# Kernel optimization log

Measured on AMD Instinct MI355X. Metric: run time of the kernel, lower is better.

Reference implementation:

```python
import jax, jax.numpy as jnp
import numpy as np

KERNEL_SIZES = (3, 5, 7)
NUM_HEAD = 6
DIM = 192
K_SCALES = 3
HEADS_PER_SCALE = NUM_HEAD // K_SCALES  # 2
HEAD_DIM = DIM // NUM_HEAD              # 32
SCALE = HEAD_DIM ** -0.5


def _nbr_idx(L, K):
    # NATTEN non-causal, dilation=1: window centered on query, clamped at edges.
    start = jnp.clip(jnp.arange(L) - K // 2, 0, L - K)
    return start[:, None] + jnp.arange(K)  # [L, K]


def _na3d_branch(xi, K):
    # xi: [B, D, H, W, C] with C = 3 * HEADS_PER_SCALE * HEAD_DIM
    B, D, H, W, C = xi.shape
    qkv = xi.reshape(B, D, H, W, 3, HEADS_PER_SCALE, HEAD_DIM).transpose(4, 0, 5, 1, 2, 3, 6)
    q, k, v = qkv[0] * SCALE, qkv[1], qkv[2]  # each [B, h, D, H, W, hd]

    idd, idh, idw = _nbr_idx(D, K), _nbr_idx(H, K), _nbr_idx(W, K)

    def gather(t):
        t = jnp.take(t, idd, axis=2)  # [B,h,D,K,H,W,hd]
        t = jnp.take(t, idh, axis=4)  # [B,h,D,K,H,K,W,hd]
        t = jnp.take(t, idw, axis=6)  # [B,h,D,K,H,K,W,K,hd]
        return t

    kn = gather(k)
    vn = gather(v)
    # attention logits over the K^3 neighborhood per query
    attn = jnp.einsum('bndhwc,bndihjwkc->bndhwijk', q, kn)
    attn = jax.nn.softmax(attn.reshape(B, HEADS_PER_SCALE, D, H, W, K ** 3), axis=-1)
    attn = attn.reshape(B, HEADS_PER_SCALE, D, H, W, K, K, K)
    y = jnp.einsum('bndhwijk,bndihjwkc->bndhwc', attn, vn)
    # [B,h,D,H,W,hd] -> [B,D,H,W,h*hd]
    return y.transpose(0, 2, 3, 4, 1, 5).reshape(B, D, H, W, HEADS_PER_SCALE * HEAD_DIM)


def setup_inputs() -> dict:
    key = jax.random.key(0)
    k0, k1, k2 = jax.random.split(key, 3)
    x = jax.random.normal(k0, (1, 8, 24, 24, DIM), dtype=jnp.float32)
    W_qkv = jax.random.normal(k1, (DIM, 3 * DIM), dtype=jnp.float32) * 0.02
    b_qkv = jnp.zeros((3 * DIM,), dtype=jnp.float32)
    W_proj = jax.random.normal(k2, (DIM, DIM), dtype=jnp.float32) * 0.02
    b_proj = jnp.zeros((DIM,), dtype=jnp.float32)
    return {'x': x, 'W_qkv': W_qkv, 'b_qkv': b_qkv, 'W_proj': W_proj, 'b_proj': b_proj}


def reference(x, W_qkv, b_qkv, W_proj, b_proj):
    qkv = x @ W_qkv + b_qkv  # [B,D,H,W,3*DIM]
    # torch.split with channels [DIM, DIM, DIM]
    chunks = jnp.split(qkv, K_SCALES, axis=4)
    ys = [_na3d_branch(chunks[i], KERNEL_SIZES[i]) for i in range(K_SCALES)]
    y = jnp.concatenate(ys, axis=4)  # [B,D,H,W,DIM]
    return y @ W_proj + b_proj
```

## Files before the change

### kernel.cpp

```cpp
#include <hip/hip_runtime.h>

typedef unsigned short ushort_t;
typedef unsigned int uint_t;
typedef __attribute__((ext_vector_type(8))) short short8;
typedef __attribute__((ext_vector_type(4))) float f32x4;

constexpr int DD = 8, HH = 24, WW = 24;
constexpr int NQ = DD * HH * WW;
constexpr int CIN = 192;
constexpr int CQKV = 576;
constexpr int KP = 576;
constexpr float ATT_SCALE = 0.17677669529663687f;
constexpr int NROW = DD * HH;

__device__ __forceinline__ ushort_t bf16h(float x) {
    uint_t u = __float_as_uint(x);
    u += 0x7FFFu + ((u >> 16) & 1u);
    return (ushort_t)(u >> 16);
}
__device__ __forceinline__ float bf16f(ushort_t h) {
    return __uint_as_float(((uint_t)h) << 16);
}
__device__ __forceinline__ float2 unpack2(uint_t u) {
    return make_float2(__uint_as_float(u << 16),
                       __uint_as_float(u & 0xffff0000u));
}
__device__ __forceinline__ float quad_add_xor1(float x) {
    return x + __int_as_float(__builtin_amdgcn_mov_dpp(__float_as_int(x), 0xB1, 0xF, 0xF, true));
}
__device__ __forceinline__ float quad_add_xor2(float x) {
    return x + __int_as_float(__builtin_amdgcn_mov_dpp(__float_as_int(x), 0x4E, 0xF, 0xF, true));
}

constexpr int EB0 = 0;
constexpr int EB1 = NROW * 2 * WW * 2;
constexpr int EB2 = EB1 + NROW * 3 * WW * 2;
constexpr int ETOT = EB2 + NROW * 4 * WW * 2;

__global__ __launch_bounds__(256)
void convert_w_kernel(const float* __restrict__ Wq, const float* __restrict__ Wp,
                      ushort_t* __restrict__ Bq, ushort_t* __restrict__ Bp)
{
    __shared__ float T[32][36];
    int b = blockIdx.x;
    const float* W; ushort_t* Bb; int N;
    int kt, nt;
    if (b < 108) { W = Wq; Bb = Bq; N = CQKV; kt = b % 6; nt = b / 6; }
    else         { b -= 108; W = Wp; Bb = Bp; N = CIN; kt = b % 6; nt = b / 6; }
    const int k0 = kt * 32, n0 = nt * 32;
    const int tid = threadIdx.x;

    #pragma unroll
    for (int p = 0; p < 4; ++p) {
        int e = p * 256 + tid;
        int r = e >> 5, c = e & 31;
        T[c][r] = W[(long)(k0 + r) * N + n0 + c];
    }
    __syncthreads();
    const int n = tid >> 3;
    const int k4 = (tid & 7) * 4;
    float4 v = *(const float4*)(&T[n][k4]);
    ushort4 hv, lv;
    hv.x = bf16h(v.x); lv.x = bf16h(v.x - bf16f(hv.x));
    hv.y = bf16h(v.y); lv.y = bf16h(v.y - bf16f(hv.y));
    hv.z = bf16h(v.z); lv.z = bf16h(v.z - bf16f(hv.z));
    hv.w = bf16h(v.w); lv.w = bf16h(v.w - bf16f(hv.w));
    const int k = k0 + k4;
    const int g = k >> 6;
    const int kc = k & 63;
    ushort_t* row = Bb + (long)(n0 + n) * KP + g * 192 + kc;
    *(ushort4*)(row)       = hv;
    *(ushort4*)(row + 64)  = lv;
    *(ushort4*)(row + 128) = hv;
}

__global__ __launch_bounds__(256)
void gemm_mfma_kernel(const float* __restrict__ A, const ushort_t* __restrict__ Bb,
                      const float* __restrict__ bias, ushort_t* __restrict__ Cout, int N)
{
    __shared__ ushort_t As[64][72];
    __shared__ ushort_t Bs[64][72];
    __shared__ float Ct[64][68];

    const int tid = threadIdx.x;
    const int bm = blockIdx.x * 64;
    const int bn = blockIdx.y * 64;

    const int wv = tid >> 6;
    const int lane = tid & 63;
    const int lm = lane & 15;
    const int quad = lane >> 4;
    const int wr = (wv >> 1) * 32;
    const int wc = (wv & 1) * 32;

    const int ar = tid >> 4;
    const int ac4 = (tid & 15) * 4;
    const int br0 = tid >> 3;
    const int bc0 = (tid & 7) * 8;

    f32x4 acc[2][2] = {};

    float4 av[4];
    #pragma unroll
    for (int p = 0; p < 4; ++p)
        av[p] = *(const float4*)(A + (long)(bm + ar + p * 16) * CIN + ac4);
    uint4 nb0 = *(const uint4*)(Bb + (long)(bn + br0) * KP + bc0);
    uint4 nb1 = *(const uint4*)(Bb + (long)(bn + br0 + 32) * KP + bc0);

    #pragma unroll
    for (int g = 0; g < 3; ++g) {
        ushort4 hv4[4];
        #pragma unroll
        for (int ph = 0; ph < 3; ++ph) {
            const uint4 b0 = nb0, b1 = nb1;
            __syncthreads();
            if (ph == 0) {
                #pragma unroll
                for (int p = 0; p < 4; ++p) {
                    float4 v = av[p];
                    ushort4 hv;
                    hv.x = bf16h(v.x); hv.y = bf16h(v.y);
                    hv.z = bf16h(v.z); hv.w = bf16h(v.w);
                    hv4[p] = hv;
                    *(ushort4*)(&As[ar + p * 16][ac4]) = hv;
                }
            } else if (ph == 2) {
                #pragma unroll
                for (int p = 0; p < 4; ++p) {
                    float4 v = av[p];
                    ushort4 lv;
                    lv.x = bf16h(v.x - bf16f(hv4[p].x));
                    lv.y = bf16h(v.y - bf16f(hv4[p].y));
                    lv.z = bf16h(v.z - bf16f(hv4[p].z));
                    lv.w = bf16h(v.w - bf16f(hv4[p].w));
                    *(ushort4*)(&As[ar + p * 16][ac4]) = lv;
                }
            }
            *(uint4*)(&Bs[br0][bc0]) = b0;
            *(uint4*)(&Bs[br0 + 32][bc0]) = b1;
            const int nidx = g * 3 + ph + 1;
            if (nidx < 9) {
                const int nkk = (nidx / 3) * 192 + (nidx % 3) * 64;
                nb0 = *(const uint4*)(Bb + (long)(bn + br0) * KP + nkk + bc0);
                nb1 = *(const uint4*)(Bb + (long)(bn + br0 + 32) * KP + nkk + bc0);
            }
            if (ph == 2 && g < 2) {
                #pragma unroll
                for (int p = 0; p < 4; ++p)
                    av[p] = *(const float4*)(A + (long)(bm + ar + p * 16) * CIN + (g + 1) * 64 + ac4);
            }
            __syncthreads();

            #pragma unroll
            for (int ks = 0; ks < 64; ks += 32) {
                short8 af0 = *(const short8*)(&As[wr + lm][ks + quad * 8]);
                short8 af1 = *(const short8*)(&As[wr + 16 + lm][ks + quad * 8]);
                short8 bf0 = *(const short8*)(&Bs[wc + lm][ks + quad * 8]);
                short8 bf1 = *(const short8*)(&Bs[wc + 16 + lm][ks + quad * 8]);
                acc[0][0] = __builtin_amdgcn_mfma_f32_16x16x32_bf16(af0, bf0, acc[0][0], 0, 0, 0);
                acc[0][1] = __builtin_amdgcn_mfma_f32_16x16x32_bf16(af0, bf1, acc[0][1], 0, 0, 0);
                acc[1][0] = __builtin_amdgcn_mfma_f32_16x16x32_bf16(af1, bf0, acc[1][0], 0, 0, 0);
                acc[1][1] = __builtin_amdgcn_mfma_f32_16x16x32_bf16(af1, bf1, acc[1][1], 0, 0, 0);
            }
        }
    }

    #pragma unroll
    for (int tc = 0; tc < 2; ++tc) {
        const float bv = bias[bn + wc + tc * 16 + lm];
        #pragma unroll
        for (int tr = 0; tr < 2; ++tr) {
            #pragma unroll
            for (int reg = 0; reg < 4; ++reg)
                Ct[wr + tr * 16 + quad * 4 + reg][wc + tc * 16 + lm] = acc[tr][tc][reg] + bv;
        }
    }
    __syncthreads();
    const int orow = tid >> 4;
    const int oc4 = (tid & 15) * 4;
    #pragma unroll
    for (int p = 0; p < 4; ++p) {
        const int r = orow + p * 16;
        float4 v = *(const float4*)(&Ct[r][oc4]);
        ushort4 hv;
        hv.x = bf16h(v.x); hv.y = bf16h(v.y); hv.z = bf16h(v.z); hv.w = bf16h(v.w);
        *(ushort4*)(Cout + (long)(bm + r) * N + bn + oc4) = hv;
    }
}

__global__ __launch_bounds__(256)
void gemm_proj_kernel(const float* __restrict__ accs, const float* __restrict__ stats,
                      const ushort_t* __restrict__ Bb, const float* __restrict__ bias,
                      float* __restrict__ Cout)
{
    __shared__ ushort_t As[64][72];
    __shared__ ushort_t Bs[64][72];
    __shared__ float Ct[64][68];

    const int tid = threadIdx.x;
    const int bm = blockIdx.x * 64;
    const int bn = blockIdx.y * 64;

    const int wv = tid >> 6;
    const int lane = tid & 63;
    const int lm = lane & 15;
    const int quad = lane >> 4;
    const int wr = (wv >> 1) * 32;
    const int wc = (wv & 1) * 32;

    const int ar = tid >> 4;
    const int ac4 = (tid & 15) * 4;
    const int a_hd = ac4 >> 5;
    const int a_cc = ac4 & 31;
    const int br0 = tid >> 3;
    const int bc0 = (tid & 7) * 8;

    f32x4 acc[2][2] = {};

    auto load_av = [&](int gg, float4* av) {
        const int CK = gg + 2;
        const int eb = (gg == 0) ? EB0 : (gg == 1 ? EB1 : EB2);
        #pragma unroll
        for (int p = 0; p < 4; ++p) {
            const int q = bm + ar + p * 16;
            const int rr = q / WW;
            const int w = q - rr * WW;
            const int e0 = eb + (rr * CK) * (WW * 2) + w * 2 + a_hd;
            float S = 0.f;
            float4 a = make_float4(0.f, 0.f, 0.f, 0.f);
            #pragma unroll
            for (int c = 0; c < 4; ++c) {
                if (c < CK) {
                    const int e = e0 + c * (WW * 2);
                    S += stats[e];
                    const float4 t = *(const float4*)(accs + (long)e * 32 + a_cc);
                    a.x += t.x; a.y += t.y; a.z += t.z; a.w += t.w;
                }
            }
            const float rs = 1.0f / S;
            av[p] = make_float4(a.x * rs, a.y * rs, a.z * rs, a.w * rs);
        }
    };

    float4 av[4];
    load_av(0, av);
    uint4 nb0 = *(const uint4*)(Bb + (long)(bn + br0) * KP + bc0);
    uint4 nb1 = *(const uint4*)(Bb + (long)(bn + br0 + 32) * KP + bc0);

    #pragma unroll
    for (int g = 0; g < 3; ++g) {
        ushort4 hv4[4];
        #pragma unroll
        for (int ph = 0; ph < 3; ++ph) {
            const uint4 b0 = nb0, b1 = nb1;
            __syncthreads();
            if (ph == 0) {
                #pragma unroll
                for (int p = 0; p < 4; ++p) {
                    float4 v = av[p];
                    ushort4 hv;
                    hv.x = bf16h(v.x); hv.y = bf16h(v.y);
                    hv.z = bf16h(v.z); hv.w = bf16h(v.w);
                    hv4[p] = hv;
                    *(ushort4*)(&As[ar + p * 16][ac4]) = hv;
                }
            } else if (ph == 2) {
                #pragma unroll
                for (int p = 0; p < 4; ++p) {
                    float4 v = av[p];
                    ushort4 lv;
                    lv.x = bf16h(v.x - bf16f(hv4[p].x));
                    lv.y = bf16h(v.y - bf16f(hv4[p].y));
                    lv.z = bf16h(v.z - bf16f(hv4[p].z));
                    lv.w = bf16h(v.w - bf16f(hv4[p].w));
                    *(ushort4*)(&As[ar + p * 16][ac4]) = lv;
                }
            }
            *(uint4*)(&Bs[br0][bc0]) = b0;
            *(uint4*)(&Bs[br0 + 32][bc0]) = b1;
            const int nidx = g * 3 + ph + 1;
            if (nidx < 9) {
                const int nkk = (nidx / 3) * 192 + (nidx % 3) * 64;
                nb0 = *(const uint4*)(Bb + (long)(bn + br0) * KP + nkk + bc0);
                nb1 = *(const uint4*)(Bb + (long)(bn + br0 + 32) * KP + nkk + bc0);
            }
            if (ph == 2 && g < 2)
                load_av(g + 1, av);
            __syncthreads();

            #pragma unroll
            for (int ks = 0; ks < 64; ks += 32) {
                short8 af0 = *(const short8*)(&As[wr + lm][ks + quad * 8]);
                short8 af1 = *(const short8*)(&As[wr + 16 + lm][ks + quad * 8]);
                short8 bf0 = *(const short8*)(&Bs[wc + lm][ks + quad * 8]);
                short8 bf1 = *(const short8*)(&Bs[wc + 16 + lm][ks + quad * 8]);
                acc[0][0] = __builtin_amdgcn_mfma_f32_16x16x32_bf16(af0, bf0, acc[0][0], 0, 0, 0);
                acc[0][1] = __builtin_amdgcn_mfma_f32_16x16x32_bf16(af0, bf1, acc[0][1], 0, 0, 0);
                acc[1][0] = __builtin_amdgcn_mfma_f32_16x16x32_bf16(af1, bf0, acc[1][0], 0, 0, 0);
                acc[1][1] = __builtin_amdgcn_mfma_f32_16x16x32_bf16(af1, bf1, acc[1][1], 0, 0, 0);
            }
        }
    }

    #pragma unroll
    for (int tc = 0; tc < 2; ++tc) {
        const float bv = bias[bn + wc + tc * 16 + lm];
        #pragma unroll
        for (int tr = 0; tr < 2; ++tr) {
            #pragma unroll
            for (int reg = 0; reg < 4; ++reg)
                Ct[wr + tr * 16 + quad * 4 + reg][wc + tc * 16 + lm] = acc[tr][tc][reg] + bv;
        }
    }
    __syncthreads();
    const int orow = tid >> 4;
    const int oc4 = (tid & 15) * 4;
    #pragma unroll
    for (int p = 0; p < 4; ++p) {
        const int r = orow + p * 16;
        float4 v = *(const float4*)(&Ct[r][oc4]);
        *(float4*)(Cout + (long)(bm + r) * CIN + bn + oc4) = v;
    }
}

constexpr int KROW = 72;
constexpr int RBUF = WW * KROW;

template<int K>
__device__ __forceinline__
void split_chunk(const ushort_t* __restrict__ qkv,
                 float* __restrict__ accs, float* __restrict__ stats,
                 int r, int c, int nchunks, int scale, int ebase,
                 int w, int hd, int d8, int tid,
                 ushort_t* __restrict__ ksh, ushort_t* __restrict__ vsh)
{
    const int i0 = 2 * c;
    const int ni = (K - i0) < 2 ? (K - i0) : 2;
    const int NT = ni * K;

    const int dq = r / HH, hq = r % HH;
    int sd = dq - K / 2; sd = sd < 0 ? 0 : (sd > DD - K ? DD - K : sd);
    int sh = hq - K / 2; sh = sh < 0 ? 0 : (sh > HH - K ? HH - K : sh);
    int sw = w  - K / 2; sw = sw < 0 ? 0 : (sw > WW - K ? WW - K : sw);

    const int q = (dq * HH + hq) * WW + w;

    uint4 qu = *(const uint4*)(qkv + (long)q * CQKV + scale * 192 + hd * 32 + d8 * 8);
    float2 qf[4] = {unpack2(qu.x), unpack2(qu.y), unpack2(qu.z), unpack2(qu.w)};
    #pragma unroll
    for (int t = 0; t < 4; ++t) {
        qf[t].x *= ATT_SCALE;
        qf[t].y *= ATT_SCALE;
    }

    const int lw = tid >> 3;
    const int c8 = (tid & 7) * 8;

    auto src_ptr = [&](int t) {
        int i = i0 + t / K;
        int j = t - (t / K) * K;
        return qkv + (long)(((sd + i) * HH + (sh + j)) * WW + lw) * CQKV
             + scale * 192 + c8;
    };

    uint4 ck, cv;
    {
        const ushort_t* p0 = src_ptr(0);
        uint4 k0 = *(const uint4*)(p0 + 64);
        uint4 v0 = *(const uint4*)(p0 + 128);
        const ushort_t* p1 = src_ptr(1);
        ck = *(const uint4*)(p1 + 64);
        cv = *(const uint4*)(p1 + 128);
        *(uint4*)(ksh + lw * KROW + c8) = k0;
        *(uint4*)(vsh + lw * KROW + c8) = v0;
    }

    float sum = 0.f;
    float2 acc[4] = {};
    const int choff = hd * 32 + d8 * 8;

    for (int t = 0; t < NT; ++t) {
        __syncthreads();
        uint4 nk, nv;
        const bool issue = (t + 2 < NT);
        if (issue) {
            const ushort_t* pn = src_ptr(t + 2);
            nk = *(const uint4*)(pn + 64);
            nv = *(const uint4*)(pn + 128);
        }

        const ushort_t* kb = ksh + (t % 3) * RBUF + choff;
        const ushort_t* vb = vsh + (t % 3) * RBUF + choff;
        #pragma unroll
        for (int n = 0; n < K; ++n) {
            uint4 ku = *(const uint4*)(kb + (sw + n) * KROW);
            float2 k0 = unpack2(ku.x), k1 = unpack2(ku.y),
                   k2 = unpack2(ku.z), k3 = unpack2(ku.w);
            float2 d;
            d.x  = qf[0].x * k0.x; d.y  = qf[0].y * k0.y;
            d.x += qf[1].x * k1.x; d.y += qf[1].y * k1.y;
            d.x += qf[2].x * k2.x; d.y += qf[2].y * k2.y;
            d.x += qf[3].x * k3.x; d.y += qf[3].y * k3.y;
            float p = d.x + d.y;
            p = quad_add_xor1(p);
            p = quad_add_xor2(p);
            float pr = __expf(p);
            sum += pr;
            uint4 vu = *(const uint4*)(vb + (sw + n) * KROW);
            float2 v0 = unpack2(vu.x), v1 = unpack2(vu.y),
                   v2 = unpack2(vu.z), v3 = unpack2(vu.w);
            acc[0].x += pr * v0.x; acc[0].y += pr * v0.y;
            acc[1].x += pr * v1.x; acc[1].y += pr * v1.y;
            acc[2].x += pr * v2.x; acc[2].y += pr * v2.y;
            acc[3].x += pr * v3.x; acc[3].y += pr * v3.y;
        }

        if (t + 1 < NT) {
            *(uint4*)(ksh + ((t + 1) % 3) * RBUF + lw * KROW + c8) = ck;
            *(uint4*)(vsh + ((t + 1) % 3) * RBUF + lw * KROW + c8) = cv;
        }
        ck = nk; cv = nv;
    }

    const int e = ebase + ((r * nchunks + c) * WW + w) * 2 + hd;
    if (d8 == 0) stats[e] = sum;
    float* ap = accs + (long)e * 32 + d8 * 8;
    *(float4*)(ap)     = make_float4(acc[0].x, acc[0].y, acc[1].x, acc[1].y);
    *(float4*)(ap + 4) = make_float4(acc[2].x, acc[2].y, acc[3].x, acc[3].y);
}

__global__ __launch_bounds__(192)
void na3d_split_kernel(const ushort_t* __restrict__ qkv,
                       float* __restrict__ accs, float* __restrict__ stats)
{
    __shared__ alignas(16) ushort_t ksh[3 * RBUF];
    __shared__ alignas(16) ushort_t vsh[3 * RBUF];

    const int tid = threadIdx.x;
    const int w  = tid >> 3;
    const int hd = (tid >> 2) & 1;
    const int d8 = tid & 3;

    const int orig = blockIdx.x;
    int bid;
    if (orig < NROW * 4) {
        bid = (orig & 7) * (NROW * 4 / 8) + (orig >> 3);
    } else if (orig < NROW * 7) {
        const int t = orig - NROW * 4;
        bid = NROW * 4 + (t & 7) * (NROW * 3 / 8) + (t >> 3);
    } else {
        const int t = orig - NROW * 7;
        bid = NROW * 7 + (t & 7) * (NROW * 2 / 8) + (t >> 3);
    }

    if (bid < NROW * 4) {
        int r = bid >> 2, c = bid & 3;
        split_chunk<7>(qkv, accs, stats, r, c, 4, 2, EB2, w, hd, d8, tid, ksh, vsh);
    } else if (bid < NROW * 4 + NROW * 3) {
        int t = bid - NROW * 4;
        int r = t / 3, c = t - (t / 3) * 3;
        split_chunk<5>(qkv, accs, stats, r, c, 3, 1, EB1, w, hd, d8, tid, ksh, vsh);
    } else {
        int t = bid - NROW * 7;
        int r = t >> 1, c = t & 1;
        split_chunk<3>(qkv, accs, stats, r, c, 2, 0, EB0, w, hd, d8, tid, ksh, vsh);
    }
}

extern "C" void kernel_launch(void* const* d_in, const int* in_sizes, int n_in,
                              void* d_out, int out_size, void* d_ws, size_t ws_size,
                              hipStream_t stream)
{
    const float* x      = (const float*)d_in[0];
    const float* W_qkv  = (const float*)d_in[1];
    const float* b_qkv  = (const float*)d_in[2];
    const float* W_proj = (const float*)d_in[3];
    const float* b_proj = (const float*)d_in[4];
    float* out = (float*)d_out;

    float* accs    = (float*)d_ws;
    float* stats   = accs + (long)ETOT * 32;
    ushort_t* qkvb = (ushort_t*)(stats + ETOT);
    ushort_t* Wbq  = qkvb + (long)NQ * CQKV;
    ushort_t* Wbp  = Wbq + (long)CQKV * KP;

    convert_w_kernel<<<dim3(144), 256, 0, stream>>>(W_qkv, W_proj, Wbq, Wbp);

    gemm_mfma_kernel<<<dim3(NQ / 64, CQKV / 64), 256, 0, stream>>>(x, Wbq, b_qkv, qkvb, CQKV);

    na3d_split_kernel<<<dim3(NROW * (4 + 3 + 2)), 192, 0, stream>>>(qkvb, accs, stats);

    gemm_proj_kernel<<<dim3(NQ / 64, CIN / 64), 256, 0, stream>>>(accs, stats, Wbp, b_proj, out);
}
```

Before: 110.4 us.

## Fuse weight conversion into QKV GEMM and use fp16 dot2 in attention

```diff
diff --git a/kernel.cpp b/kernel.cpp
--- a/kernel.cpp
+++ b/kernel.cpp
@@ -3,7 +3,9 @@
 typedef unsigned short ushort_t;
 typedef unsigned int uint_t;
 typedef __attribute__((ext_vector_type(8))) short short8;
+typedef __attribute__((ext_vector_type(8))) unsigned short ushort8;
 typedef __attribute__((ext_vector_type(4))) float f32x4;
+typedef __attribute__((ext_vector_type(2))) _Float16 half2v;
 
 constexpr int DD = 8, HH = 24, WW = 24;
 constexpr int NQ = DD * HH * WW;
@@ -21,9 +23,9 @@
 __device__ __forceinline__ float bf16f(ushort_t h) {
     return __uint_as_float(((uint_t)h) << 16);
 }
-__device__ __forceinline__ float2 unpack2(uint_t u) {
-    return make_float2(__uint_as_float(u << 16),
-                       __uint_as_float(u & 0xffff0000u));
+__device__ __forceinline__ ushort_t f16h(float x) {
+    _Float16 h = (_Float16)x;
+    return __builtin_bit_cast(ushort_t, h);
 }
 __device__ __forceinline__ float quad_add_xor1(float x) {
     return x + __int_as_float(__builtin_amdgcn_mov_dpp(__float_as_int(x), 0xB1, 0xF, 0xF, true));
@@ -38,133 +40,164 @@
 constexpr int ETOT = EB2 + NROW * 4 * WW * 2;
 
 __global__ __launch_bounds__(256)
-void convert_w_kernel(const float* __restrict__ Wq, const float* __restrict__ Wp,
-                      ushort_t* __restrict__ Bq, ushort_t* __restrict__ Bp)
-{
-    __shared__ float T[32][36];
-    int b = blockIdx.x;
-    const float* W; ushort_t* Bb; int N;
-    int kt, nt;
-    if (b < 108) { W = Wq; Bb = Bq; N = CQKV; kt = b % 6; nt = b / 6; }
-    else         { b -= 108; W = Wp; Bb = Bp; N = CIN; kt = b % 6; nt = b / 6; }
-    const int k0 = kt * 32, n0 = nt * 32;
-    const int tid = threadIdx.x;
-
-    #pragma unroll
-    for (int p = 0; p < 4; ++p) {
-        int e = p * 256 + tid;
-        int r = e >> 5, c = e & 31;
-        T[c][r] = W[(long)(k0 + r) * N + n0 + c];
-    }
-    __syncthreads();
-    const int n = tid >> 3;
-    const int k4 = (tid & 7) * 4;
-    float4 v = *(const float4*)(&T[n][k4]);
-    ushort4 hv, lv;
-    hv.x = bf16h(v.x); lv.x = bf16h(v.x - bf16f(hv.x));
-    hv.y = bf16h(v.y); lv.y = bf16h(v.y - bf16f(hv.y));
-    hv.z = bf16h(v.z); lv.z = bf16h(v.z - bf16f(hv.z));
-    hv.w = bf16h(v.w); lv.w = bf16h(v.w - bf16f(hv.w));
-    const int k = k0 + k4;
-    const int g = k >> 6;
-    const int kc = k & 63;
-    ushort_t* row = Bb + (long)(n0 + n) * KP + g * 192 + kc;
-    *(ushort4*)(row)       = hv;
-    *(ushort4*)(row + 64)  = lv;
-    *(ushort4*)(row + 128) = hv;
-}
-
-__global__ __launch_bounds__(256)
-void gemm_mfma_kernel(const float* __restrict__ A, const ushort_t* __restrict__ Bb,
-                      const float* __restrict__ bias, ushort_t* __restrict__ Cout, int N)
+void gemm_qkv_kernel(const float* __restrict__ A, const float* __restrict__ Wq,
+                     const float* __restrict__ bias, const float* __restrict__ Wp,
+                     ushort_t* __restrict__ Cout, ushort_t* __restrict__ Bp)
 {
     __shared__ ushort_t As[64][72];
-    __shared__ ushort_t Bs[64][72];
-    __shared__ float Ct[64][68];
-
+    __shared__ ushort_t Bh[64][72];
+    __shared__ ushort_t Bl[64][72];
+    __shared__ float CS[64][68];
+
+    const int bx = blockIdx.x;
     const int tid = threadIdx.x;
-    const int bm = blockIdx.x * 64;
-    const int bn = blockIdx.y * 64;
-
-    const int wv = tid >> 6;
+
+    if (bx >= 648) {
+        float (*T)[36] = (float(*)[36])CS;
+        const int b = bx - 648;
+        const int kt = b % 6, nt = b / 6;
+        const int k0 = kt * 32, n0 = nt * 32;
+        #pragma unroll
+        for (int p = 0; p < 4; ++p) {
+            int e = p * 256 + tid;
+            int r = e >> 5, c = e & 31;
+            T[c][r] = Wp[(long)(k0 + r) * CIN + n0 + c];
+        }
+        __syncthreads();
+        const int n = tid >> 3;
+        const int k4 = (tid & 7) * 4;
+        float4 v = *(const float4*)(&T[n][k4]);
+        ushort4 hv, lv;
+        hv.x = bf16h(v.x); lv.x = bf16h(v.x - bf16f(hv.x));
+        hv.y = bf16h(v.y); lv.y = bf16h(v.y - bf16f(hv.y));
+        hv.z = bf16h(v.z); lv.z = bf16h(v.z - bf16f(hv.z));
+        hv.w = bf16h(v.w); lv.w = bf16h(v.w - bf16f(hv.w));
+        const int k = k0 + k4;
+        const int g = k >> 6;
+        const int kc = k & 63;
+        ushort_t* row = Bp + (long)(n0 + n) * KP + g * 192 + kc;
+        *(ushort4*)(row)       = hv;
+        *(ushort4*)(row + 64)  = lv;
+        *(ushort4*)(row + 128) = hv;
+        return;
+    }
+
+    const int bm = (bx % 72) * 64;
+    const int bn = (bx / 72) * 64;
+
+    const int wv_ = tid >> 6;
     const int lane = tid & 63;
     const int lm = lane & 15;
     const int quad = lane >> 4;
-    const int wr = (wv >> 1) * 32;
-    const int wc = (wv & 1) * 32;
+    const int wr = (wv_ >> 1) * 32;
+    const int wc = (wv_ & 1) * 32;
 
     const int ar = tid >> 4;
     const int ac4 = (tid & 15) * 4;
-    const int br0 = tid >> 3;
-    const int bc0 = (tid & 7) * 8;
+    const int kr = tid >> 4;
+    const int nc4 = (tid & 15) * 4;
+    const int bni = tid & 63;
+    const int ks16 = (tid >> 6) * 16;
 
     f32x4 acc[2][2] = {};
 
-    float4 av[4];
-    #pragma unroll
-    for (int p = 0; p < 4; ++p)
-        av[p] = *(const float4*)(A + (long)(bm + ar + p * 16) * CIN + ac4);
-    uint4 nb0 = *(const uint4*)(Bb + (long)(bn + br0) * KP + bc0);
-    uint4 nb1 = *(const uint4*)(Bb + (long)(bn + br0 + 32) * KP + bc0);
+    float4 av[4], wv4[4];
+    #pragma unroll
+    for (int p = 0; p < 4; ++p) {
+        av[p]  = *(const float4*)(A  + (long)(bm + ar + p * 16) * CIN  + ac4);
+        wv4[p] = *(const float4*)(Wq + (long)(kr + p * 16)      * CQKV + bn + nc4);
+    }
 
     #pragma unroll
     for (int g = 0; g < 3; ++g) {
         ushort4 hv4[4];
         #pragma unroll
-        for (int ph = 0; ph < 3; ++ph) {
-            const uint4 b0 = nb0, b1 = nb1;
-            __syncthreads();
-            if (ph == 0) {
-                #pragma unroll
-                for (int p = 0; p < 4; ++p) {
-                    float4 v = av[p];
-                    ushort4 hv;
-                    hv.x = bf16h(v.x); hv.y = bf16h(v.y);
-                    hv.z = bf16h(v.z); hv.w = bf16h(v.w);
-                    hv4[p] = hv;
-                    *(ushort4*)(&As[ar + p * 16][ac4]) = hv;
-                }
-            } else if (ph == 2) {
-                #pragma unroll
-                for (int p = 0; p < 4; ++p) {
-                    float4 v = av[p];
-                    ushort4 lv;
-                    lv.x = bf16h(v.x - bf16f(hv4[p].x));
-                    lv.y = bf16h(v.y - bf16f(hv4[p].y));
-                    lv.z = bf16h(v.z - bf16f(hv4[p].z));
-                    lv.w = bf16h(v.w - bf16f(hv4[p].w));
-                    *(ushort4*)(&As[ar + p * 16][ac4]) = lv;
-                }
+        for (int p = 0; p < 4; ++p) {
+            *(float4*)(&CS[kr + p * 16][nc4]) = wv4[p];
+            float4 v = av[p];
+            ushort4 hv;
+            hv.x = bf16h(v.x); hv.y = bf16h(v.y);
+            hv.z = bf16h(v.z); hv.w = bf16h(v.w);
+            hv4[p] = hv;
+            *(ushort4*)(&As[ar + p * 16][ac4]) = hv;
+        }
+        __syncthreads();
+
+        {
+            ushort8 hr0, hr1, lr0, lr1;
+            #pragma unroll
+            for (int j = 0; j < 8; ++j) {
+                float f0 = CS[ks16 + j][bni];
+                ushort_t h0 = bf16h(f0);
+                hr0[j] = h0;
+                lr0[j] = bf16h(f0 - bf16f(h0));
+                float f1 = CS[ks16 + 8 + j][bni];
+                ushort_t h1 = bf16h(f1);
+                hr1[j] = h1;
+                lr1[j] = bf16h(f1 - bf16f(h1));
             }
-            *(uint4*)(&Bs[br0][bc0]) = b0;
-            *(uint4*)(&Bs[br0 + 32][bc0]) = b1;
-            const int nidx = g * 3 + ph + 1;
-            if (nidx < 9) {
-                const int nkk = (nidx / 3) * 192 + (nidx % 3) * 64;
-                nb0 = *(const uint4*)(Bb + (long)(bn + br0) * KP + nkk + bc0);
-                nb1 = *(const uint4*)(Bb + (long)(bn + br0 + 32) * KP + nkk + bc0);
+            *(ushort8*)(&Bh[bni][ks16])     = hr0;
+            *(ushort8*)(&Bh[bni][ks16 + 8]) = hr1;
+            *(ushort8*)(&Bl[bni][ks16])     = lr0;
+            *(ushort8*)(&Bl[bni][ks16 + 8]) = lr1;
+        }
+        __syncthreads();
+
+        ushort4 lv4[4];
+        #pragma unroll
+        for (int p = 0; p < 4; ++p) {
+            float4 v = av[p];
+            lv4[p].x = bf16h(v.x - bf16f(hv4[p].x));
+            lv4[p].y = bf16h(v.y - bf16f(hv4[p].y));
+            lv4[p].z = bf16h(v.z - bf16f(hv4[p].z));
+            lv4[p].w = bf16h(v.w - bf16f(hv4[p].w));
+        }
+        if (g < 2) {
+            #pragma unroll
+            for (int p = 0; p < 4; ++p) {
+                av[p]  = *(const float4*)(A  + (long)(bm + ar + p * 16) * CIN  + (g + 1) * 64 + ac4);
+                wv4[p] = *(const float4*)(Wq + (long)((g + 1) * 64 + kr + p * 16) * CQKV + bn + nc4);
             }
-            if (ph == 2 && g < 2) {
-                #pragma unroll
-                for (int p = 0; p < 4; ++p)
-                    av[p] = *(const float4*)(A + (long)(bm + ar + p * 16) * CIN + (g + 1) * 64 + ac4);
-            }
-            __syncthreads();
-
-            #pragma unroll
-            for (int ks = 0; ks < 64; ks += 32) {
-                short8 af0 = *(const short8*)(&As[wr + lm][ks + quad * 8]);
-                short8 af1 = *(const short8*)(&As[wr + 16 + lm][ks + quad * 8]);
-                short8 bf0 = *(const short8*)(&Bs[wc + lm][ks + quad * 8]);
-                short8 bf1 = *(const short8*)(&Bs[wc + 16 + lm][ks + quad * 8]);
-                acc[0][0] = __builtin_amdgcn_mfma_f32_16x16x32_bf16(af0, bf0, acc[0][0], 0, 0, 0);
-                acc[0][1] = __builtin_amdgcn_mfma_f32_16x16x32_bf16(af0, bf1, acc[0][1], 0, 0, 0);
-                acc[1][0] = __builtin_amdgcn_mfma_f32_16x16x32_bf16(af1, bf0, acc[1][0], 0, 0, 0);
-                acc[1][1] = __builtin_amdgcn_mfma_f32_16x16x32_bf16(af1, bf1, acc[1][1], 0, 0, 0);
-            }
-        }
-    }
-
+        }
+        #pragma unroll
+        for (int ks = 0; ks < 64; ks += 32) {
+            short8 af0 = *(const short8*)(&As[wr + lm][ks + quad * 8]);
+            short8 af1 = *(const short8*)(&As[wr + 16 + lm][ks + quad * 8]);
+            short8 bh0 = *(const short8*)(&Bh[wc + lm][ks + quad * 8]);
+            short8 bh1 = *(const short8*)(&Bh[wc + 16 + lm][ks + quad * 8]);
+            short8 bl0 = *(const short8*)(&Bl[wc + lm][ks + quad * 8]);
+            short8 bl1 = *(const short8*)(&Bl[wc + 16 + lm][ks + quad * 8]);
+            acc[0][0] = __builtin_amdgcn_mfma_f32_16x16x32_bf16(af0, bh0, acc[0][0], 0, 0, 0);
+            acc[0][1] = __builtin_amdgcn_mfma_f32_16x16x32_bf16(af0, bh1, acc[0][1], 0, 0, 0);
+            acc[1][0] = __builtin_amdgcn_mfma_f32_16x16x32_bf16(af1, bh0, acc[1][0], 0, 0, 0);
+            acc[1][1] = __builtin_amdgcn_mfma_f32_16x16x32_bf16(af1, bh1, acc[1][1], 0, 0, 0);
+            acc[0][0] = __builtin_amdgcn_mfma_f32_16x16x32_bf16(af0, bl0, acc[0][0], 0, 0, 0);
+            acc[0][1] = __builtin_amdgcn_mfma_f32_16x16x32_bf16(af0, bl1, acc[0][1], 0, 0, 0);
+            acc[1][0] = __builtin_amdgcn_mfma_f32_16x16x32_bf16(af1, bl0, acc[1][0], 0, 0, 0);
+            acc[1][1] = __builtin_amdgcn_mfma_f32_16x16x32_bf16(af1, bl1, acc[1][1], 0, 0, 0);
+        }
+        __syncthreads();
+
+        #pragma unroll
+        for (int p = 0; p < 4; ++p)
+            *(ushort4*)(&As[ar + p * 16][ac4]) = lv4[p];
+        __syncthreads();
+
+        #pragma unroll
+        for (int ks = 0; ks < 64; ks += 32) {
+            short8 af0 = *(const short8*)(&As[wr + lm][ks + quad * 8]);
+            short8 af1 = *(const short8*)(&As[wr + 16 + lm][ks + quad * 8]);
+            short8 bh0 = *(const short8*)(&Bh[wc + lm][ks + quad * 8]);
+            short8 bh1 = *(const short8*)(&Bh[wc + 16 + lm][ks + quad * 8]);
+            acc[0][0] = __builtin_amdgcn_mfma_f32_16x16x32_bf16(af0, bh0, acc[0][0], 0, 0, 0);
+            acc[0][1] = __builtin_amdgcn_mfma_f32_16x16x32_bf16(af0, bh1, acc[0][1], 0, 0, 0);
+            acc[1][0] = __builtin_amdgcn_mfma_f32_16x16x32_bf16(af1, bh0, acc[1][0], 0, 0, 0);
+            acc[1][1] = __builtin_amdgcn_mfma_f32_16x16x32_bf16(af1, bh1, acc[1][1], 0, 0, 0);
+        }
+        __syncthreads();
+    }
+
+    float (*Ct)[68] = CS;
     #pragma unroll
     for (int tc = 0; tc < 2; ++tc) {
         const float bv = bias[bn + wc + tc * 16 + lm];
@@ -183,8 +216,8 @@
         const int r = orow + p * 16;
         float4 v = *(const float4*)(&Ct[r][oc4]);
         ushort4 hv;
-        hv.x = bf16h(v.x); hv.y = bf16h(v.y); hv.z = bf16h(v.z); hv.w = bf16h(v.w);
-        *(ushort4*)(Cout + (long)(bm + r) * N + bn + oc4) = hv;
+        hv.x = f16h(v.x); hv.y = f16h(v.y); hv.z = f16h(v.z); hv.w = f16h(v.w);
+        *(ushort4*)(Cout + (long)(bm + r) * CQKV + bn + oc4) = hv;
     }
 }
 
@@ -346,12 +379,8 @@
     const int q = (dq * HH + hq) * WW + w;
 
     uint4 qu = *(const uint4*)(qkv + (long)q * CQKV + scale * 192 + hd * 32 + d8 * 8);
-    float2 qf[4] = {unpack2(qu.x), unpack2(qu.y), unpack2(qu.z), unpack2(qu.w)};
-    #pragma unroll
-    for (int t = 0; t < 4; ++t) {
-        qf[t].x *= ATT_SCALE;
-        qf[t].y *= ATT_SCALE;
-    }
+    const half2v* qh = (const half2v*)&qu;
+    half2v q2[4] = {qh[0], qh[1], qh[2], qh[3]};
 
     const int lw = tid >> 3;
     const int c8 = (tid & 7) * 8;
@@ -376,7 +405,8 @@
     }
 
     float sum = 0.f;
-    float2 acc[4] = {};
+    float a0 = 0.f, a1 = 0.f, a2 = 0.f, a3 = 0.f,
+          a4 = 0.f, a5 = 0.f, a6 = 0.f, a7 = 0.f;
     const int choff = hd * 32 + d8 * 8;
 
     for (int t = 0; t < NT; ++t) {
@@ -394,25 +424,25 @@
         #pragma unroll
         for (int n = 0; n < K; ++n) {
             uint4 ku = *(const uint4*)(kb + (sw + n) * KROW);
-            float2 k0 = unpack2(ku.x), k1 = unpack2(ku.y),
-                   k2 = unpack2(ku.z), k3 = unpack2(ku.w);
-            float2 d;
-            d.x  = qf[0].x * k0.x; d.y  = qf[0].y * k0.y;
-            d.x += qf[1].x * k1.x; d.y += qf[1].y * k1.y;
-            d.x += qf[2].x * k2.x; d.y += qf[2].y * k2.y;
-            d.x += qf[3].x * k3.x; d.y += qf[3].y * k3.y;
-            float p = d.x + d.y;
-            p = quad_add_xor1(p);
+            const half2v* kh = (const half2v*)&ku;
+            float d = __builtin_amdgcn_fdot2(q2[0], kh[0], 0.0f, false);
+            d = __builtin_amdgcn_fdot2(q2[1], kh[1], d, false);
+            d = __builtin_amdgcn_fdot2(q2[2], kh[2], d, false);
+            d = __builtin_amdgcn_fdot2(q2[3], kh[3], d, false);
+            float p = quad_add_xor1(d);
             p = quad_add_xor2(p);
-            float pr = __expf(p);
+            float pr = __expf(p * ATT_SCALE);
             sum += pr;
             uint4 vu = *(const uint4*)(vb + (sw + n) * KROW);
-            float2 v0 = unpack2(vu.x), v1 = unpack2(vu.y),
-                   v2 = unpack2(vu.z), v3 = unpack2(vu.w);
-            acc[0].x += pr * v0.x; acc[0].y += pr * v0.y;
-            acc[1].x += pr * v1.x; acc[1].y += pr * v1.y;
-            acc[2].x += pr * v2.x; acc[2].y += pr * v2.y;
-            acc[3].x += pr * v3.x; acc[3].y += pr * v3.y;
+            const half2v* vh = (const half2v*)&vu;
+            a0 = fmaf(pr, (float)vh[0][0], a0);
+            a1 = fmaf(pr, (float)vh[0][1], a1);
+            a2 = fmaf(pr, (float)vh[1][0], a2);
+            a3 = fmaf(pr, (float)vh[1][1], a3);
+            a4 = fmaf(pr, (float)vh[2][0], a4);
+            a5 = fmaf(pr, (float)vh[2][1], a5);
+            a6 = fmaf(pr, (float)vh[3][0], a6);
+            a7 = fmaf(pr, (float)vh[3][1], a7);
         }
 
         if (t + 1 < NT) {
@@ -425,8 +455,8 @@
     const int e = ebase + ((r * nchunks + c) * WW + w) * 2 + hd;
     if (d8 == 0) stats[e] = sum;
     float* ap = accs + (long)e * 32 + d8 * 8;
-    *(float4*)(ap)     = make_float4(acc[0].x, acc[0].y, acc[1].x, acc[1].y);
-    *(float4*)(ap + 4) = make_float4(acc[2].x, acc[2].y, acc[3].x, acc[3].y);
+    *(float4*)(ap)     = make_float4(a0, a1, a2, a3);
+    *(float4*)(ap + 4) = make_float4(a4, a5, a6, a7);
 }
 
 __global__ __launch_bounds__(192)
@@ -481,12 +511,9 @@
     float* accs    = (float*)d_ws;
     float* stats   = accs + (long)ETOT * 32;
     ushort_t* qkvb = (ushort_t*)(stats + ETOT);
-    ushort_t* Wbq  = qkvb + (long)NQ * CQKV;
-    ushort_t* Wbp  = Wbq + (long)CQKV * KP;
-
-    convert_w_kernel<<<dim3(144), 256, 0, stream>>>(W_qkv, W_proj, Wbq, Wbp);
-
-    gemm_mfma_kernel<<<dim3(NQ / 64, CQKV / 64), 256, 0, stream>>>(x, Wbq, b_qkv, qkvb, CQKV);
+    ushort_t* Wbp  = qkvb + (long)NQ * CQKV;
+
+    gemm_qkv_kernel<<<dim3(648 + 36), 256, 0, stream>>>(x, W_qkv, b_qkv, W_proj, qkvb, Wbp);
 
     na3d_split_kernel<<<dim3(NROW * (4 + 3 + 2)), 192, 0, stream>>>(qkvb, accs, stats);
 
```

Measured after the change: 112.6 us. 2.1% more time.

## Switch GEMMs to fp16 split-A with single fp16 weights and exp2 softmax

Applied to the files above, without the earlier changes.

```diff
diff --git a/kernel.cpp b/kernel.cpp
--- a/kernel.cpp
+++ b/kernel.cpp
@@ -2,15 +2,15 @@
 
 typedef unsigned short ushort_t;
 typedef unsigned int uint_t;
-typedef __attribute__((ext_vector_type(8))) short short8;
+typedef __attribute__((ext_vector_type(8))) _Float16 half8;
 typedef __attribute__((ext_vector_type(4))) float f32x4;
 
 constexpr int DD = 8, HH = 24, WW = 24;
 constexpr int NQ = DD * HH * WW;
 constexpr int CIN = 192;
 constexpr int CQKV = 576;
-constexpr int KP = 576;
-constexpr float ATT_SCALE = 0.17677669529663687f;
+constexpr int KW = 192;
+constexpr float SCALE_LOG2E = 0.17677669529663687f * 1.4426950408889634f;
 constexpr int NROW = DD * HH;
 
 __device__ __forceinline__ ushort_t bf16h(float x) {
@@ -18,12 +18,16 @@
     u += 0x7FFFu + ((u >> 16) & 1u);
     return (ushort_t)(u >> 16);
 }
-__device__ __forceinline__ float bf16f(ushort_t h) {
-    return __uint_as_float(((uint_t)h) << 16);
-}
 __device__ __forceinline__ float2 unpack2(uint_t u) {
     return make_float2(__uint_as_float(u << 16),
                        __uint_as_float(u & 0xffff0000u));
+}
+__device__ __forceinline__ ushort_t f16h(float x) {
+    _Float16 h = (_Float16)x;
+    return __builtin_bit_cast(ushort_t, h);
+}
+__device__ __forceinline__ float f16f(ushort_t h) {
+    return (float)__builtin_bit_cast(_Float16, h);
 }
 __device__ __forceinline__ float quad_add_xor1(float x) {
     return x + __int_as_float(__builtin_amdgcn_mov_dpp(__float_as_int(x), 0xB1, 0xF, 0xF, true));
@@ -60,18 +64,9 @@
     const int n = tid >> 3;
     const int k4 = (tid & 7) * 4;
     float4 v = *(const float4*)(&T[n][k4]);
-    ushort4 hv, lv;
-    hv.x = bf16h(v.x); lv.x = bf16h(v.x - bf16f(hv.x));
-    hv.y = bf16h(v.y); lv.y = bf16h(v.y - bf16f(hv.y));
-    hv.z = bf16h(v.z); lv.z = bf16h(v.z - bf16f(hv.z));
-    hv.w = bf16h(v.w); lv.w = bf16h(v.w - bf16f(hv.w));
-    const int k = k0 + k4;
-    const int g = k >> 6;
-    const int kc = k & 63;
-    ushort_t* row = Bb + (long)(n0 + n) * KP + g * 192 + kc;
-    *(ushort4*)(row)       = hv;
-    *(ushort4*)(row + 64)  = lv;
-    *(ushort4*)(row + 128) = hv;
+    ushort4 hv;
+    hv.x = f16h(v.x); hv.y = f16h(v.y); hv.z = f16h(v.z); hv.w = f16h(v.w);
+    *(ushort4*)(Bb + (long)(n0 + n) * KW + k0 + k4) = hv;
 }
 
 __global__ __launch_bounds__(256)
@@ -104,64 +99,65 @@
     #pragma unroll
     for (int p = 0; p < 4; ++p)
         av[p] = *(const float4*)(A + (long)(bm + ar + p * 16) * CIN + ac4);
-    uint4 nb0 = *(const uint4*)(Bb + (long)(bn + br0) * KP + bc0);
-    uint4 nb1 = *(const uint4*)(Bb + (long)(bn + br0 + 32) * KP + bc0);
+    uint4 nb0 = *(const uint4*)(Bb + (long)(bn + br0) * KW + bc0);
+    uint4 nb1 = *(const uint4*)(Bb + (long)(bn + br0 + 32) * KW + bc0);
 
     #pragma unroll
     for (int g = 0; g < 3; ++g) {
-        ushort4 hv4[4];
-        #pragma unroll
-        for (int ph = 0; ph < 3; ++ph) {
-            const uint4 b0 = nb0, b1 = nb1;
-            __syncthreads();
-            if (ph == 0) {
-                #pragma unroll
-                for (int p = 0; p < 4; ++p) {
-                    float4 v = av[p];
-                    ushort4 hv;
-                    hv.x = bf16h(v.x); hv.y = bf16h(v.y);
-                    hv.z = bf16h(v.z); hv.w = bf16h(v.w);
-                    hv4[p] = hv;
-                    *(ushort4*)(&As[ar + p * 16][ac4]) = hv;
-                }
-            } else if (ph == 2) {
-                #pragma unroll
-                for (int p = 0; p < 4; ++p) {
-                    float4 v = av[p];
-                    ushort4 lv;
-                    lv.x = bf16h(v.x - bf16f(hv4[p].x));
-                    lv.y = bf16h(v.y - bf16f(hv4[p].y));
-                    lv.z = bf16h(v.z - bf16f(hv4[p].z));
-                    lv.w = bf16h(v.w - bf16f(hv4[p].w));
-                    *(ushort4*)(&As[ar + p * 16][ac4]) = lv;
-                }
-            }
-            *(uint4*)(&Bs[br0][bc0]) = b0;
-            *(uint4*)(&Bs[br0 + 32][bc0]) = b1;
-            const int nidx = g * 3 + ph + 1;
-            if (nidx < 9) {
-                const int nkk = (nidx / 3) * 192 + (nidx % 3) * 64;
-                nb0 = *(const uint4*)(Bb + (long)(bn + br0) * KP + nkk + bc0);
-                nb1 = *(const uint4*)(Bb + (long)(bn + br0 + 32) * KP + nkk + bc0);
-            }
-            if (ph == 2 && g < 2) {
-                #pragma unroll
-                for (int p = 0; p < 4; ++p)
-                    av[p] = *(const float4*)(A + (long)(bm + ar + p * 16) * CIN + (g + 1) * 64 + ac4);
-            }
-            __syncthreads();
-
+        const uint4 b0 = nb0, b1 = nb1;
+        ushort4 hv4[4], lv4[4];
+        #pragma unroll
+        for (int p = 0; p < 4; ++p) {
+            float4 v = av[p];
+            hv4[p].x = f16h(v.x); hv4[p].y = f16h(v.y);
+            hv4[p].z = f16h(v.z); hv4[p].w = f16h(v.w);
+            lv4[p].x = f16h(v.x - f16f(hv4[p].x));
+            lv4[p].y = f16h(v.y - f16f(hv4[p].y));
+            lv4[p].z = f16h(v.z - f16f(hv4[p].z));
+            lv4[p].w = f16h(v.w - f16f(hv4[p].w));
+        }
+        __syncthreads();
+        #pragma unroll
+        for (int p = 0; p < 4; ++p)
+            *(ushort4*)(&As[ar + p * 16][ac4]) = hv4[p];
+        *(uint4*)(&Bs[br0][bc0])      = b0;
+        *(uint4*)(&Bs[br0 + 32][bc0]) = b1;
+        if (g < 2) {
+            const int kk = (g + 1) * 64;
+            nb0 = *(const uint4*)(Bb + (long)(bn + br0) * KW + kk + bc0);
+            nb1 = *(const uint4*)(Bb + (long)(bn + br0 + 32) * KW + kk + bc0);
             #pragma unroll
-            for (int ks = 0; ks < 64; ks += 32) {
-                short8 af0 = *(const short8*)(&As[wr + lm][ks + quad * 8]);
-                short8 af1 = *(const short8*)(&As[wr + 16 + lm][ks + quad * 8]);
-                short8 bf0 = *(const short8*)(&Bs[wc + lm][ks + quad * 8]);
-                short8 bf1 = *(const short8*)(&Bs[wc + 16 + lm][ks + quad * 8]);
-                acc[0][0] = __builtin_amdgcn_mfma_f32_16x16x32_bf16(af0, bf0, acc[0][0], 0, 0, 0);
-                acc[0][1] = __builtin_amdgcn_mfma_f32_16x16x32_bf16(af0, bf1, acc[0][1], 0, 0, 0);
-                acc[1][0] = __builtin_amdgcn_mfma_f32_16x16x32_bf16(af1, bf0, acc[1][0], 0, 0, 0);
-                acc[1][1] = __builtin_amdgcn_mfma_f32_16x16x32_bf16(af1, bf1, acc[1][1], 0, 0, 0);
-            }
+            for (int p = 0; p < 4; ++p)
+                av[p] = *(const float4*)(A + (long)(bm + ar + p * 16) * CIN + (g + 1) * 64 + ac4);
+        }
+        __syncthreads();
+
+        #pragma unroll
+        for (int ks = 0; ks < 64; ks += 32) {
+            half8 af0 = *(const half8*)(&As[wr + lm][ks + quad * 8]);
+            half8 af1 = *(const half8*)(&As[wr + 16 + lm][ks + quad * 8]);
+            half8 bf0 = *(const half8*)(&Bs[wc + lm][ks + quad * 8]);
+            half8 bf1 = *(const half8*)(&Bs[wc + 16 + lm][ks + quad * 8]);
+            acc[0][0] = __builtin_amdgcn_mfma_f32_16x16x32_f16(af0, bf0, acc[0][0], 0, 0, 0);
+            acc[0][1] = __builtin_amdgcn_mfma_f32_16x16x32_f16(af0, bf1, acc[0][1], 0, 0, 0);
+            acc[1][0] = __builtin_amdgcn_mfma_f32_16x16x32_f16(af1, bf0, acc[1][0], 0, 0, 0);
+            acc[1][1] = __builtin_amdgcn_mfma_f32_16x16x32_f16(af1, bf1, acc[1][1], 0, 0, 0);
+        }
+        __syncthreads();
+        #pragma unroll
+        for (int p = 0; p < 4; ++p)
+            *(ushort4*)(&As[ar + p * 16][ac4]) = lv4[p];
+        __syncthreads();
+        #pragma unroll
+        for (int ks = 0; ks < 64; ks += 32) {
+            half8 af0 = *(const half8*)(&As[wr + lm][ks + quad * 8]);
+            half8 af1 = *(const half8*)(&As[wr + 16 + lm][ks + quad * 8]);
+            half8 bf0 = *(const half8*)(&Bs[wc + lm][ks + quad * 8]);
+            half8 bf1 = *(const half8*)(&Bs[wc + 16 + lm][ks + quad * 8]);
+            acc[0][0] = __builtin_amdgcn_mfma_f32_16x16x32_f16(af0, bf0, acc[0][0], 0, 0, 0);
+            acc[0][1] = __builtin_amdgcn_mfma_f32_16x16x32_f16(af0, bf1, acc[0][1], 0, 0, 0);
+            acc[1][0] = __builtin_amdgcn_mfma_f32_16x16x32_f16(af1, bf0, acc[1][0], 0, 0, 0);
+            acc[1][1] = __builtin_amdgcn_mfma_f32_16x16x32_f16(af1, bf1, acc[1][1], 0, 0, 0);
         }
     }
 
@@ -244,61 +240,63 @@
 
     float4 av[4];
     load_av(0, av);
-    uint4 nb0 = *(const uint4*)(Bb + (long)(bn + br0) * KP + bc0);
-    uint4 nb1 = *(const uint4*)(Bb + (long)(bn + br0 + 32) * KP + bc0);
+    uint4 nb0 = *(const uint4*)(Bb + (long)(bn + br0) * KW + bc0);
+    uint4 nb1 = *(const uint4*)(Bb + (long)(bn + br0 + 32) * KW + bc0);
 
     #pragma unroll
     for (int g = 0; g < 3; ++g) {
-        ushort4 hv4[4];
-        #pragma unroll
-        for (int ph = 0; ph < 3; ++ph) {
-            const uint4 b0 = nb0, b1 = nb1;
-            __syncthreads();
-            if (ph == 0) {
-                #pragma unroll
-                for (int p = 0; p < 4; ++p) {
-                    float4 v = av[p];
-                    ushort4 hv;
-                    hv.x = bf16h(v.x); hv.y = bf16h(v.y);
-                    hv.z = bf16h(v.z); hv.w = bf16h(v.w);
-                    hv4[p] = hv;
-                    *(ushort4*)(&As[ar + p * 16][ac4]) = hv;
-                }
-            } else if (ph == 2) {
-                #pragma unroll
-                for (int p = 0; p < 4; ++p) {
-                    float4 v = av[p];
-                    ushort4 lv;
-                    lv.x = bf16h(v.x - bf16f(hv4[p].x));
-                    lv.y = bf16h(v.y - bf16f(hv4[p].y));
-                    lv.z = bf16h(v.z - bf16f(hv4[p].z));
-                    lv.w = bf16h(v.w - bf16f(hv4[p].w));
-                    *(ushort4*)(&As[ar + p * 16][ac4]) = lv;
-                }
-            }
-            *(uint4*)(&Bs[br0][bc0]) = b0;
-            *(uint4*)(&Bs[br0 + 32][bc0]) = b1;
-            const int nidx = g * 3 + ph + 1;
-            if (nidx < 9) {
-                const int nkk = (nidx / 3) * 192 + (nidx % 3) * 64;
-                nb0 = *(const uint4*)(Bb + (long)(bn + br0) * KP + nkk + bc0);
-                nb1 = *(const uint4*)(Bb + (long)(bn + br0 + 32) * KP + nkk + bc0);
-            }
-            if (ph == 2 && g < 2)
-                load_av(g + 1, av);
-            __syncthreads();
-
-            #pragma unroll
-            for (int ks = 0; ks < 64; ks += 32) {
-                short8 af0 = *(const short8*)(&As[wr + lm][ks + quad * 8]);
-                short8 af1 = *(const short8*)(&As[wr + 16 + lm][ks + quad * 8]);
-                short8 bf0 = *(const short8*)(&Bs[wc + lm][ks + quad * 8]);
-                short8 bf1 = *(const short8*)(&Bs[wc + 16 + lm][ks + quad * 8]);
-                acc[0][0] = __builtin_amdgcn_mfma_f32_16x16x32_bf16(af0, bf0, acc[0][0], 0, 0, 0);
-                acc[0][1] = __builtin_amdgcn_mfma_f32_16x16x32_bf16(af0, bf1, acc[0][1], 0, 0, 0);
-                acc[1][0] = __builtin_amdgcn_mfma_f32_16x16x32_bf16(af1, bf0, acc[1][0], 0, 0, 0);
-                acc[1][1] = __builtin_amdgcn_mfma_f32_16x16x32_bf16(af1, bf1, acc[1][1], 0, 0, 0);
-            }
+        const uint4 b0 = nb0, b1 = nb1;
+        ushort4 hv4[4], lv4[4];
+        #pragma unroll
+        for (int p = 0; p < 4; ++p) {
+            float4 v = av[p];
+            hv4[p].x = f16h(v.x); hv4[p].y = f16h(v.y);
+            hv4[p].z = f16h(v.z); hv4[p].w = f16h(v.w);
+            lv4[p].x = f16h(v.x - f16f(hv4[p].x));
+            lv4[p].y = f16h(v.y - f16f(hv4[p].y));
+            lv4[p].z = f16h(v.z - f16f(hv4[p].z));
+            lv4[p].w = f16h(v.w - f16f(hv4[p].w));
+        }
+        __syncthreads();
+        #pragma unroll
+        for (int p = 0; p < 4; ++p)
+            *(ushort4*)(&As[ar + p * 16][ac4]) = hv4[p];
+        *(uint4*)(&Bs[br0][bc0])      = b0;
+        *(uint4*)(&Bs[br0 + 32][bc0]) = b1;
+        if (g < 2) {
+            const int kk = (g + 1) * 64;
+            nb0 = *(const uint4*)(Bb + (long)(bn + br0) * KW + kk + bc0);
+            nb1 = *(const uint4*)(Bb + (long)(bn + br0 + 32) * KW + kk + bc0);
+            load_av(g + 1, av);
+        }
+        __syncthreads();
+
+        #pragma unroll
+        for (int ks = 0; ks < 64; ks += 32) {
+            half8 af0 = *(const half8*)(&As[wr + lm][ks + quad * 8]);
+            half8 af1 = *(const half8*)(&As[wr + 16 + lm][ks + quad * 8]);
+            half8 bf0 = *(const half8*)(&Bs[wc + lm][ks + quad * 8]);
+            half8 bf1 = *(const half8*)(&Bs[wc + 16 + lm][ks + quad * 8]);
+            acc[0][0] = __builtin_amdgcn_mfma_f32_16x16x32_f16(af0, bf0, acc[0][0], 0, 0, 0);
+            acc[0][1] = __builtin_amdgcn_mfma_f32_16x16x32_f16(af0, bf1, acc[0][1], 0, 0, 0);
+            acc[1][0] = __builtin_amdgcn_mfma_f32_16x16x32_f16(af1, bf0, acc[1][0], 0, 0, 0);
+            acc[1][1] = __builtin_amdgcn_mfma_f32_16x16x32_f16(af1, bf1, acc[1][1], 0, 0, 0);
+        }
+        __syncthreads();
+        #pragma unroll
+        for (int p = 0; p < 4; ++p)
+            *(ushort4*)(&As[ar + p * 16][ac4]) = lv4[p];
+        __syncthreads();
+        #pragma unroll
+        for (int ks = 0; ks < 64; ks += 32) {
+            half8 af0 = *(const half8*)(&As[wr + lm][ks + quad * 8]);
+            half8 af1 = *(const half8*)(&As[wr + 16 + lm][ks + quad * 8]);
+            half8 bf0 = *(const half8*)(&Bs[wc + lm][ks + quad * 8]);
+            half8 bf1 = *(const half8*)(&Bs[wc + 16 + lm][ks + quad * 8]);
+            acc[0][0] = __builtin_amdgcn_mfma_f32_16x16x32_f16(af0, bf0, acc[0][0], 0, 0, 0);
+            acc[0][1] = __builtin_amdgcn_mfma_f32_16x16x32_f16(af0, bf1, acc[0][1], 0, 0, 0);
+            acc[1][0] = __builtin_amdgcn_mfma_f32_16x16x32_f16(af1, bf0, acc[1][0], 0, 0, 0);
+            acc[1][1] = __builtin_amdgcn_mfma_f32_16x16x32_f16(af1, bf1, acc[1][1], 0, 0, 0);
         }
     }
 
@@ -349,8 +347,8 @@
     float2 qf[4] = {unpack2(qu.x), unpack2(qu.y), unpack2(qu.z), unpack2(qu.w)};
     #pragma unroll
     for (int t = 0; t < 4; ++t) {
-        qf[t].x *= ATT_SCALE;
-        qf[t].y *= ATT_SCALE;
+        qf[t].x *= SCALE_LOG2E;
+        qf[t].y *= SCALE_LOG2E;
     }
 
     const int lw = tid >> 3;
@@ -404,7 +402,7 @@
             float p = d.x + d.y;
             p = quad_add_xor1(p);
             p = quad_add_xor2(p);
-            float pr = __expf(p);
+            float pr = exp2f(p);
             sum += pr;
             uint4 vu = *(const uint4*)(vb + (sw + n) * KROW);
             float2 v0 = unpack2(vu.x), v1 = unpack2(vu.y),
@@ -482,7 +480,7 @@
     float* stats   = accs + (long)ETOT * 32;
     ushort_t* qkvb = (ushort_t*)(stats + ETOT);
     ushort_t* Wbq  = qkvb + (long)NQ * CQKV;
-    ushort_t* Wbp  = Wbq + (long)CQKV * KP;
+    ushort_t* Wbp  = Wbq + (long)CQKV * KW;
 
     convert_w_kernel<<<dim3(144), 256, 0, stream>>>(W_qkv, W_proj, Wbq, Wbp);
 
```

Measured after the change: 106.9 us, median of 2. 3.1% less time.
